# Kernel optimization log

Measured on AMD Instinct MI355X. Metric: run time of the kernel, lower is better.

The kernel has to match this reference:

```python
import jax, jax.numpy as jnp
import numpy as np

D_MODEL = 1024
D_HIDDEN = 4096
N_EXPERTS = 8
B, S = 2, 2048


def setup_inputs() -> dict:
    key = jax.random.key(0)
    ks = jax.random.split(key, 4)
    sd = 1.0 / np.sqrt(D_MODEL)
    sh = 1.0 / np.sqrt(D_HIDDEN)
    return {
        "x": jax.random.normal(ks[0], (B, S, D_MODEL), dtype=jnp.float32),
        "Wg": jax.random.normal(ks[1], (D_MODEL, N_EXPERTS), dtype=jnp.float32) * sd,
        "bg": jnp.zeros((N_EXPERTS,), dtype=jnp.float32),
        "W1": jax.random.normal(ks[2], (N_EXPERTS, D_MODEL, D_HIDDEN), dtype=jnp.float32) * sd,
        "b1": jnp.zeros((N_EXPERTS, D_HIDDEN), dtype=jnp.float32),
        "W2": jax.random.normal(ks[3], (N_EXPERTS, D_HIDDEN, D_MODEL), dtype=jnp.float32) * sh,
        "b2": jnp.zeros((N_EXPERTS, D_MODEL), dtype=jnp.float32),
    }


def reference(x, Wg, bg, W1, b1, W2, b2):
    # Router: softmax is monotone, so argmax(softmax(logits)) == argmax(logits).
    logits = jnp.einsum("bsd,de->bse", x, Wg) + bg
    expert_idx = jnp.argmax(logits, axis=-1)  # [B, S]
    # Top-1 dispatch, expressed as compute-all-experts + per-token select
    # (jit-friendly; the torch loop masks/gathers per expert).
    h = jax.nn.gelu(jnp.einsum("bsd,edh->bseh", x, W1) + b1, approximate=False)
    y = jnp.einsum("bseh,ehd->bsed", h, W2) + b2  # [B, S, E, D]
    out = jnp.take_along_axis(y, expert_idx[:, :, None, None], axis=2)[:, :, 0, :]
    return out
```

## Files before the change

kernel.cpp:

```cpp
#include <hip/hip_runtime.h>
#include <hip/hip_bf16.h>
#include <math.h>

#define D_MODEL 1024
#define D_HIDDEN 4096
#define N_EXP 8
#define N_TOK 4096
#define MBS2 24

typedef __attribute__((ext_vector_type(8))) __bf16 bf16x8_t;
typedef __attribute__((ext_vector_type(4))) float f32x4_t;

#define WS_PREFIX_OFF 128
#define WS_BUCKET_OFF 256
#define WS_HT_OFF     ((size_t)1 << 18)
#define WS_XB_OFF     ((size_t)1 << 18)
#define WS_HFB_OFF    (((size_t)1 << 18) + ((size_t)8 << 20))
#define WS_W1T_OFF    (((size_t)1 << 18) + ((size_t)48 << 20))
#define WS_W2T_OFF    (((size_t)1 << 18) + ((size_t)112 << 20))
#define WS_AE_OFF     (((size_t)1 << 18) + ((size_t)176 << 20))
#define WS_NEED       (((size_t)1 << 18) + ((size_t)188 << 20))

__device__ __forceinline__ void gload16(const void* g, void* l) {
    __builtin_amdgcn_global_load_lds(
        (__attribute__((address_space(1))) void*)(g),
        (__attribute__((address_space(3))) void*)(l),
        16, 0, 0);
}

__global__ __launch_bounds__(64) void init_counts(int* counts) {
    if (threadIdx.x < N_EXP) counts[threadIdx.x] = 0;
}

__global__ __launch_bounds__(64) void prefix_kernel(const int* counts, int* prefix) {
    if (threadIdx.x == 0) {
        int s = 0;
        prefix[0] = 0;
#pragma unroll
        for (int e = 0; e < N_EXP; ++e) { s += (counts[e] + 255) >> 8; prefix[e + 1] = s; }
    }
}

__global__ __launch_bounds__(256) void router_kernel(
    const float* __restrict__ x, const float* __restrict__ Wg,
    const float* __restrict__ bg, int* __restrict__ counts,
    int* __restrict__ bucket, __hip_bfloat16* __restrict__ xb)
{
    const int wid  = threadIdx.x >> 6;
    const int lane = threadIdx.x & 63;
    const int t    = blockIdx.x * 4 + wid;
    const float* xr = x + (size_t)t * D_MODEL;

    double acc[N_EXP];
#pragma unroll
    for (int e = 0; e < N_EXP; ++e) acc[e] = 0.0;

#pragma unroll
    for (int j = 0; j < D_MODEL / 64; ++j) {
        const int d = j * 64 + lane;
        const float xv = xr[d];
        xb[(size_t)t * D_MODEL + d] = __float2bfloat16(xv);
        const float4* wr = (const float4*)(Wg + (size_t)d * N_EXP);
        const float4 w0 = wr[0], w1 = wr[1];
        const double xd = (double)xv;
        acc[0] += xd * (double)w0.x; acc[1] += xd * (double)w0.y;
        acc[2] += xd * (double)w0.z; acc[3] += xd * (double)w0.w;
        acc[4] += xd * (double)w1.x; acc[5] += xd * (double)w1.y;
        acc[6] += xd * (double)w1.z; acc[7] += xd * (double)w1.w;
    }
#pragma unroll
    for (int e = 0; e < N_EXP; ++e) {
        double v = acc[e];
#pragma unroll
        for (int off = 32; off >= 1; off >>= 1) v += __shfl_xor(v, off, 64);
        acc[e] = v + (double)bg[e];
    }
    if (lane == 0) {
        int best = 0; double bv = acc[0];
#pragma unroll
        for (int e = 1; e < N_EXP; ++e)
            if (acc[e] > bv) { bv = acc[e]; best = e; }
        const int pos = atomicAdd(&counts[best], 1);
        bucket[best * N_TOK + pos] = t;
    }
}

template<int KT, int NT>
__global__ __launch_bounds__(256) void convert_w(
    const float* __restrict__ W, __hip_bfloat16* __restrict__ Wt)
{
    constexpr int NB = NT / 256, KC = KT / 64;
    const int nb128 = blockIdx.x, kc = blockIdx.y, e = blockIdx.z;
    const int k0 = kc * 64, n0 = nb128 * 128;
    const int nb = n0 >> 8, halfc = (n0 >> 7) & 1;
    const int tid = threadIdx.x;
    __shared__ __hip_bfloat16 Lt[128 * 68];

    const int nq  = tid & 31;
    const int kq2 = tid >> 5;
#pragma unroll
    for (int h = 0; h < 2; ++h) {
        const int kq = kq2 + h * 8;
        const float* src = W + (size_t)e * KT * NT + (size_t)(k0 + kq * 4) * NT + n0 + nq * 4;
        const float4 v0 = *(const float4*)(src);
        const float4 v1 = *(const float4*)(src + (size_t)NT);
        const float4 v2 = *(const float4*)(src + (size_t)2 * NT);
        const float4 v3 = *(const float4*)(src + (size_t)3 * NT);
#pragma unroll
        for (int i = 0; i < 4; ++i) {
            const int n = nq * 4 + i;
            union { __hip_bfloat16 hh[4]; unsigned long long u; } pk;
            pk.hh[0] = __float2bfloat16(((const float*)&v0)[i]);
            pk.hh[1] = __float2bfloat16(((const float*)&v1)[i]);
            pk.hh[2] = __float2bfloat16(((const float*)&v2)[i]);
            pk.hh[3] = __float2bfloat16(((const float*)&v3)[i]);
            *(unsigned long long*)((char*)Lt + (size_t)n * 136 + kq * 8) = pk.u;
        }
    }
    __syncthreads();

    char* outc = (char*)Wt + (((size_t)e * NB + nb) * KC + kc) * 32768 + halfc * 16384;
    const int n = tid >> 1, half = tid & 1;
#pragma unroll
    for (int s = 0; s < 4; ++s) {
        const int slot = half * 4 + s;
        const int ko = slot ^ (n & 7);
        const uint4 v = *(const uint4*)((const char*)Lt + (size_t)n * 136 + ko * 16);
        *(uint4*)(outc + (size_t)n * 128 + slot * 16) = v;
    }
}

__global__ __launch_bounds__(256) void gather_a(
    const float* __restrict__ x, const int* __restrict__ counts,
    const int* __restrict__ prefix, const int* __restrict__ bucket,
    __hip_bfloat16* __restrict__ Ae)
{
    const int mbg = blockIdx.x >> 1, halfm = blockIdx.x & 1, kc = blockIdx.y;
    if (mbg >= prefix[8]) return;
    int e = 0;
#pragma unroll
    for (int q = 1; q < 8; ++q) if (mbg >= prefix[q]) e = q;
    const int cnt  = counts[e];
    const int mblk = mbg - prefix[e];
    const int tid  = threadIdx.x;
    const int m = halfm * 128 + (tid >> 1);
    const int half = tid & 1;
    int idx = mblk * 256 + m;
    if (idx >= cnt) idx = cnt - 1;
    const int tok = bucket[e * N_TOK + idx];
    const float* src = x + (size_t)tok * D_MODEL + kc * 64 + half * 32;
    char* dst = (char*)Ae + ((size_t)mbg * 16 + kc) * 32768 + (size_t)m * 128;
#pragma unroll
    for (int s = 0; s < 4; ++s) {
        const float4 a = *(const float4*)(src + s * 8);
        const float4 b = *(const float4*)(src + s * 8 + 4);
        union { __hip_bfloat16 hh[8]; uint4 u; } pk;
#pragma unroll
        for (int j = 0; j < 4; ++j) {
            pk.hh[j]     = __float2bfloat16(((const float*)&a)[j]);
            pk.hh[j + 4] = __float2bfloat16(((const float*)&b)[j]);
        }
        const int ko = half * 4 + s;
        *(uint4*)(dst + ((ko ^ (m & 7)) << 4)) = pk.u;
    }
}

template<int K_TOT, int N_TOT, int SPLITS, bool IS_FFN1>
__global__ __launch_bounds__(512, 2) void ffn_gemm_q(
    const __hip_bfloat16* __restrict__ At,
    const __hip_bfloat16* __restrict__ Wt,
    const float* __restrict__ bias,
    const int* __restrict__ prefix,
    __hip_bfloat16* __restrict__ hout,
    float* __restrict__ pout)
{
    constexpr int KC     = K_TOT / 64;
    constexpr int KSTEPS = KC / SPLITS;
    constexpr int NB     = N_TOT / 256;
    constexpr int NWG    = NB * SPLITS * MBS2;

    const int orig = blockIdx.x;
    const int wg   = (orig & 7) * (NWG >> 3) + (orig >> 3);
    const int nblk = wg / (SPLITS * MBS2);
    const int r2   = wg % (SPLITS * MBS2);
    const int split = r2 / MBS2;
    const int mbg   = r2 % MBS2;
    if (mbg >= prefix[8]) return;
    int e = 0;
#pragma unroll
    for (int q = 1; q < 8; ++q) if (mbg >= prefix[q]) e = q;
    const int n0 = nblk * 256;

    const int tid  = threadIdx.x;
    const int lane = tid & 63;
    const int wid  = tid >> 6;
    const int wm   = wid >> 1, wn = wid & 1;

    __shared__ char As[2 * 32768];
    __shared__ char Bs[2 * 32768];

    const char* Ab = (const char*)At + ((size_t)mbg * KC + split * KSTEPS) * 32768;
    const char* Bb = (const char*)Wt + (((size_t)e * NB + nblk) * KC + split * KSTEPS) * 32768;
    const int off = wid * 4096 + lane * 16;
    char* lA = As + wid * 4096;
    char* lB = Bs + wid * 4096;

    f32x4_t acc[4][8];
#pragma unroll
    for (int f = 0; f < 4; ++f)
#pragma unroll
        for (int g = 0; g < 8; ++g) acc[f][g] = (f32x4_t){0.f, 0.f, 0.f, 0.f};

    {
        const char* Ac = Ab + off;
        const char* Bc = Bb + off;
#pragma unroll
        for (int i = 0; i < 4; ++i) gload16(Ac + i * 1024, lA + i * 1024);
#pragma unroll
        for (int i = 0; i < 4; ++i) gload16(Bc + i * 1024, lB + i * 1024);
    }
    asm volatile("s_waitcnt vmcnt(0)" ::: "memory");
    __builtin_amdgcn_s_barrier();
    __builtin_amdgcn_sched_barrier(0);

    for (int t = 0; t < KSTEPS; ++t) {
        const int c = t & 1;
        if (t + 1 < KSTEPS) {
            const char* Ac = Ab + (size_t)(t + 1) * 32768 + off;
            const char* Bc = Bb + (size_t)(t + 1) * 32768 + off;
            char* la = lA + (c ^ 1) * 32768;
            char* lb = lB + (c ^ 1) * 32768;
#pragma unroll
            for (int i = 0; i < 4; ++i) gload16(Ac + i * 1024, la + i * 1024);
#pragma unroll
            for (int i = 0; i < 4; ++i) gload16(Bc + i * 1024, lb + i * 1024);
        }
        __builtin_amdgcn_sched_barrier(0);

        const char* asb = As + c * 32768;
        const char* bsb = Bs + c * 32768;
#pragma unroll
        for (int kk = 0; kk < 2; ++kk) {
            uint4 af[4], bf[8];
            const int ko = kk * 4 + (lane >> 4);
#pragma unroll
            for (int f = 0; f < 4; ++f) {
                const int r = wm * 64 + f * 16 + (lane & 15);
                af[f] = *(const uint4*)(asb + r * 128 + ((ko ^ (r & 7)) << 4));
            }
#pragma unroll
            for (int g = 0; g < 8; ++g) {
                const int n = wn * 128 + g * 16 + (lane & 15);
                bf[g] = *(const uint4*)(bsb + n * 128 + ((ko ^ (n & 7)) << 4));
            }
#pragma unroll
            for (int f = 0; f < 4; ++f)
#pragma unroll
                for (int g = 0; g < 8; ++g)
                    acc[f][g] = __builtin_amdgcn_mfma_f32_16x16x32_bf16(
                        __builtin_bit_cast(bf16x8_t, af[f]),
                        __builtin_bit_cast(bf16x8_t, bf[g]),
                        acc[f][g], 0, 0, 0);
        }

        asm volatile("s_waitcnt vmcnt(0)" ::: "memory");
        __builtin_amdgcn_s_barrier();
        __builtin_amdgcn_sched_barrier(0);
    }

    if (IS_FFN1) {
        char* hb = (char*)hout + (size_t)mbg * (D_HIDDEN / 64) * 32768;
#pragma unroll
        for (int f = 0; f < 4; ++f) {
#pragma unroll
            for (int j = 0; j < 4; ++j) {
                const int m = wm * 64 + f * 16 + (lane >> 4) * 4 + j;
#pragma unroll
                for (int g = 0; g < 8; ++g) {
                    const int col = n0 + wn * 128 + g * 16 + (lane & 15);
                    float v = acc[f][g][j] + bias[e * N_TOT + col];
                    v = 0.5f * v * (1.0f + erff(v * 0.70710678118654752f));
                    const int kc = col >> 6, kw = col & 63, ko = kw >> 3, b = kw & 7;
                    *(__hip_bfloat16*)(hb + (size_t)kc * 32768 + (size_t)m * 128 +
                                       (((ko ^ (m & 7)) << 4) + (b << 1))) = __float2bfloat16(v);
                }
            }
        }
    } else {
        float* pb = pout + ((size_t)(split * MBS2 + mbg) * 256) * 1024;
#pragma unroll
        for (int f = 0; f < 4; ++f) {
#pragma unroll
            for (int j = 0; j < 4; ++j) {
                const int m = wm * 64 + f * 16 + (lane >> 4) * 4 + j;
#pragma unroll
                for (int g = 0; g < 8; ++g) {
                    const int col = n0 + wn * 128 + g * 16 + (lane & 15);
                    pb[(size_t)m * 1024 + col] = acc[f][g][j];
                }
            }
        }
    }
}

__global__ __launch_bounds__(256) void reduce_out(
    const float* __restrict__ P, const float* __restrict__ b2,
    const int* __restrict__ counts, const int* __restrict__ prefix,
    const int* __restrict__ bucket, float* __restrict__ out)
{
    const int slot = blockIdx.x;
    if (slot >= prefix[8]) return;
    int e = 0;
#pragma unroll
    for (int q = 1; q < 8; ++q) if (slot >= prefix[q]) e = q;
    const int cnt  = counts[e];
    const int mblk = slot - prefix[e];
    const int r    = blockIdx.y * 4 + (threadIdx.x >> 6);
    const int idx  = mblk * 256 + r;
    if (idx >= cnt) return;
    const int tok  = bucket[e * N_TOK + idx];
    const int lane = threadIdx.x & 63;
    const float* p0 = P + ((size_t)slot * 256 + r) * 1024;
    const float* p1 = P + ((size_t)(MBS2 + slot) * 256 + r) * 1024;
    const float* bb = b2 + e * 1024;
    float* op = out + (size_t)tok * 1024;
#pragma unroll
    for (int j = 0; j < 4; ++j) {
        const int c = j * 256 + lane * 4;
        const float4 a = *(const float4*)(p0 + c);
        const float4 b = *(const float4*)(p1 + c);
        const float4 w = *(const float4*)(bb + c);
        float4 v;
        v.x = a.x + b.x + w.x; v.y = a.y + b.y + w.y;
        v.z = a.z + b.z + w.z; v.w = a.w + b.w + w.w;
        *(float4*)(op + c) = v;
    }
}

template<int K_TOT, int N_TOT, bool IS_FFN1>
__global__ __launch_bounds__(256, 2) void ffn_gemm_f32(
    const __hip_bfloat16* __restrict__ A,
    const float* __restrict__ W,
    const float* __restrict__ bias,
    const int* __restrict__ counts,
    const int* __restrict__ bucket,
    __hip_bfloat16* __restrict__ hout,
    float* __restrict__ yout)
{
    const int e   = blockIdx.z;
    const int cnt = counts[e];
    const int m0  = blockIdx.y * 128;
    if (m0 >= cnt) return;
    const int n0   = blockIdx.x * 128;
    const int tid  = threadIdx.x;
    const int lane = tid & 63;
    const int wid  = tid >> 6;
    const int wm   = wid >> 1, wn = wid & 1;

    __shared__ __hip_bfloat16 As[128 * 64];
    __shared__ __hip_bfloat16 Bs[128 * 64];
    __shared__ int s_tok[128];

    if (tid < 128) {
        int idx = m0 + tid;
        if (idx >= cnt) idx = cnt - 1;
        s_tok[tid] = bucket[e * N_TOK + idx];
    }
    __syncthreads();

    const __hip_bfloat16* gA[4]; char* lA[4];
#pragma unroll
    for (int i = 0; i < 4; ++i) {
        const int r = wid * 32 + i * 8 + (lane >> 3);
        gA[i] = A + (size_t)s_tok[r] * K_TOT + (((lane & 7) ^ (r & 7)) << 3);
        lA[i] = (char*)As + (size_t)(wid * 32 + i * 8) * 128;
    }
    const int ko_t = lane & 7;
    const int nq   = wid * 8 + (lane >> 3);
    const float* wb = W + (size_t)e * K_TOT * N_TOT + (size_t)(ko_t * 8) * N_TOT + n0 + nq * 4;

    f32x4_t acc[4][4];
#pragma unroll
    for (int f = 0; f < 4; ++f)
#pragma unroll
        for (int g = 0; g < 4; ++g) acc[f][g] = (f32x4_t){0.f, 0.f, 0.f, 0.f};

    for (int k0 = 0; k0 < K_TOT; k0 += 64) {
#pragma unroll
        for (int i = 0; i < 4; ++i) gload16(gA[i] + k0, lA[i]);
        const float* wk = wb + (size_t)k0 * N_TOT;
        float4 v[8];
#pragma unroll
        for (int j = 0; j < 8; ++j) v[j] = *(const float4*)(wk + (size_t)j * N_TOT);
#pragma unroll
        for (int i = 0; i < 4; ++i) {
            const int n = nq * 4 + i;
            union { __hip_bfloat16 hh[8]; uint4 u; } pk;
#pragma unroll
            for (int j = 0; j < 8; ++j) pk.hh[j] = __float2bfloat16(((const float*)&v[j])[i]);
            *(uint4*)((char*)Bs + n * 128 + ((ko_t ^ (n & 7)) << 4)) = pk.u;
        }
        __syncthreads();

#pragma unroll
        for (int kk = 0; kk < 2; ++kk) {
            uint4 af[4], bf[4];
            const int ko = kk * 4 + (lane >> 4);
#pragma unroll
            for (int f = 0; f < 4; ++f) {
                const int r = wm * 64 + f * 16 + (lane & 15);
                af[f] = *(const uint4*)((const char*)As + r * 128 + ((ko ^ (r & 7)) << 4));
            }
#pragma unroll
            for (int g = 0; g < 4; ++g) {
                const int n = wn * 64 + g * 16 + (lane & 15);
                bf[g] = *(const uint4*)((const char*)Bs + n * 128 + ((ko ^ (n & 7)) << 4));
            }
#pragma unroll
            for (int f = 0; f < 4; ++f)
#pragma unroll
                for (int g = 0; g < 4; ++g)
                    acc[f][g] = __builtin_amdgcn_mfma_f32_16x16x32_bf16(
                        __builtin_bit_cast(bf16x8_t, af[f]),
                        __builtin_bit_cast(bf16x8_t, bf[g]),
                        acc[f][g], 0, 0, 0);
        }
        __syncthreads();
    }

#pragma unroll
    for (int f = 0; f < 4; ++f) {
#pragma unroll
        for (int j = 0; j < 4; ++j) {
            const int rl = wm * 64 + f * 16 + (lane >> 4) * 4 + j;
            const bool ok = (m0 + rl) < cnt;
            const int tok = s_tok[rl];
#pragma unroll
            for (int g = 0; g < 4; ++g) {
                const int col = n0 + wn * 64 + g * 16 + (lane & 15);
                float v = acc[f][g][j] + bias[e * N_TOT + col];
                if (IS_FFN1) {
                    v = 0.5f * v * (1.0f + erff(v * 0.70710678118654752f));
                    if (ok) hout[(size_t)tok * N_TOT + col] = __float2bfloat16(v);
                } else {
                    if (ok) yout[(size_t)tok * N_TOT + col] = v;
                }
            }
        }
    }
}

extern "C" void kernel_launch(void* const* d_in, const int* in_sizes, int n_in,
                              void* d_out, int out_size, void* d_ws, size_t ws_size,
                              hipStream_t stream) {
    const float* x  = (const float*)d_in[0];
    const float* Wg = (const float*)d_in[1];
    const float* bg = (const float*)d_in[2];
    const float* W1 = (const float*)d_in[3];
    const float* b1 = (const float*)d_in[4];
    const float* W2 = (const float*)d_in[5];
    const float* b2 = (const float*)d_in[6];
    float* out = (float*)d_out;

    char* ws = (char*)d_ws;
    int* counts = (int*)(ws);
    int* prefix = (int*)(ws + WS_PREFIX_OFF);
    int* bucket = (int*)(ws + WS_BUCKET_OFF);
    __hip_bfloat16* xb  = (__hip_bfloat16*)(ws + WS_XB_OFF);
    __hip_bfloat16* ht  = (__hip_bfloat16*)(ws + WS_HT_OFF);
    __hip_bfloat16* hfb = (__hip_bfloat16*)(ws + WS_HFB_OFF);
    __hip_bfloat16* w1t = (__hip_bfloat16*)(ws + WS_W1T_OFF);
    __hip_bfloat16* w2t = (__hip_bfloat16*)(ws + WS_W2T_OFF);
    __hip_bfloat16* ae  = (__hip_bfloat16*)(ws + WS_AE_OFF);
    float* partials     = (float*)(ws + WS_W1T_OFF);

    init_counts<<<dim3(1), dim3(64), 0, stream>>>(counts);
    router_kernel<<<dim3(N_TOK / 4), dim3(256), 0, stream>>>(x, Wg, bg, counts, bucket, xb);
    prefix_kernel<<<dim3(1), dim3(64), 0, stream>>>(counts, prefix);

    if (ws_size >= WS_NEED) {
        convert_w<D_MODEL, D_HIDDEN><<<dim3(32, 16, N_EXP), dim3(256), 0, stream>>>(W1, w1t);
        convert_w<D_HIDDEN, D_MODEL><<<dim3(8, 64, N_EXP), dim3(256), 0, stream>>>(W2, w2t);
        gather_a<<<dim3(MBS2 * 2, 16), dim3(256), 0, stream>>>(x, counts, prefix, bucket, ae);
        ffn_gemm_q<D_MODEL, D_HIDDEN, 1, true>
            <<<dim3(MBS2 * (D_HIDDEN / 256)), dim3(512), 0, stream>>>(
                ae, w1t, b1, prefix, ht, nullptr);
        ffn_gemm_q<D_HIDDEN, D_MODEL, 2, false>
            <<<dim3(MBS2 * (D_MODEL / 256) * 2), dim3(512), 0, stream>>>(
                ht, w2t, nullptr, prefix, nullptr, partials);
        reduce_out<<<dim3(MBS2, 64), dim3(256), 0, stream>>>(
            partials, b2, counts, prefix, bucket, out);
    } else {
        ffn_gemm_f32<D_MODEL, D_HIDDEN, true>
            <<<dim3(D_HIDDEN / 128, N_TOK / 128, N_EXP), dim3(256), 0, stream>>>(
                xb, W1, b1, counts, bucket, hfb, nullptr);
        ffn_gemm_f32<D_HIDDEN, D_MODEL, false>
            <<<dim3(D_MODEL / 128, N_TOK / 128, N_EXP), dim3(256), 0, stream>>>(
                hfb, W2, b2, counts, bucket, nullptr, out);
    }
}
```

Baseline: 354.8 us.

## Halve GEMM K-tile to 32 and raise occupancy to four blocks per CU

Changes the pre-tiled bf16 layout of the weights, the gathered activations and the hidden buffer from 64-wide to 32-wide K chunks, with a new 4-slot XOR swizzle. The GEMM now uses 64KB of LDS instead of 128KB and does one MFMA k-step per pipeline stage, and launch bounds ask for 4 blocks per CU instead of 2. The aim is more resident workgroups to hide memory latency. In exchange it adds twice as many barriers and waits per unit of K, and it may cause register spills under the tighter register budget with 32 accumulator vectors per thread.

```diff
diff --git a/kernel.cpp b/kernel.cpp
--- a/kernel.cpp
+++ b/kernel.cpp
@@ -89,10 +89,10 @@
 __global__ __launch_bounds__(256) void convert_w(
     const float* __restrict__ W, __hip_bfloat16* __restrict__ Wt)
 {
-    constexpr int NB = NT / 256, KC = KT / 64;
+    constexpr int NB = NT / 256, KC2 = KT / 32;
     const int nb128 = blockIdx.x, kc = blockIdx.y, e = blockIdx.z;
     const int k0 = kc * 64, n0 = nb128 * 128;
-    const int nb = n0 >> 8, halfc = (n0 >> 7) & 1;
+    const int nb = nb128 >> 1, roff = (nb128 & 1) * 128;
     const int tid = threadIdx.x;
     __shared__ __hip_bfloat16 Lt[128 * 68];
 
@@ -119,14 +119,14 @@
     }
     __syncthreads();
 
-    char* outc = (char*)Wt + (((size_t)e * NB + nb) * KC + kc) * 32768 + halfc * 16384;
     const int n = tid >> 1, half = tid & 1;
+    const int m = roff + n;
+    char* outc = (char*)Wt + (((size_t)e * NB + nb) * KC2 + kc * 2 + half) * 16384;
 #pragma unroll
     for (int s = 0; s < 4; ++s) {
-        const int slot = half * 4 + s;
-        const int ko = slot ^ (n & 7);
-        const uint4 v = *(const uint4*)((const char*)Lt + (size_t)n * 136 + ko * 16);
-        *(uint4*)(outc + (size_t)n * 128 + slot * 16) = v;
+        const int phys = s ^ ((m >> 1) & 3);
+        const uint4 v = *(const uint4*)((const char*)Lt + (size_t)n * 136 + half * 64 + s * 16);
+        *(uint4*)(outc + (size_t)m * 64 + phys * 16) = v;
     }
 }
 
@@ -149,7 +149,7 @@
     if (idx >= cnt) idx = cnt - 1;
     const int tok = bucket[e * N_TOK + idx];
     const float* src = x + (size_t)tok * D_MODEL + kc * 64 + half * 32;
-    char* dst = (char*)Ae + ((size_t)mbg * 16 + kc) * 32768 + (size_t)m * 128;
+    char* dst = (char*)Ae + ((size_t)mbg * 32 + kc * 2 + half) * 16384 + (size_t)m * 64;
 #pragma unroll
     for (int s = 0; s < 4; ++s) {
         const float4 a = *(const float4*)(src + s * 8);
@@ -160,13 +160,13 @@
             pk.hh[j]     = __float2bfloat16(((const float*)&a)[j]);
             pk.hh[j + 4] = __float2bfloat16(((const float*)&b)[j]);
         }
-        const int ko = half * 4 + s;
-        *(uint4*)(dst + ((ko ^ (m & 7)) << 4)) = pk.u;
+        const int phys = s ^ ((m >> 1) & 3);
+        *(uint4*)(dst + phys * 16) = pk.u;
     }
 }
 
 template<int K_TOT, int N_TOT, int SPLITS, bool IS_FFN1>
-__global__ __launch_bounds__(512, 2) void ffn_gemm_q(
+__global__ __launch_bounds__(512, 4) void ffn_gemm_q(
     const __hip_bfloat16* __restrict__ At,
     const __hip_bfloat16* __restrict__ Wt,
     const float* __restrict__ bias,
@@ -174,8 +174,8 @@
     __hip_bfloat16* __restrict__ hout,
     float* __restrict__ pout)
 {
-    constexpr int KC     = K_TOT / 64;
-    constexpr int KSTEPS = KC / SPLITS;
+    constexpr int KC2    = K_TOT / 32;
+    constexpr int KSTEPS = KC2 / SPLITS;
     constexpr int NB     = N_TOT / 256;
     constexpr int NWG    = NB * SPLITS * MBS2;
 
@@ -196,14 +196,14 @@
     const int wid  = tid >> 6;
     const int wm   = wid >> 1, wn = wid & 1;
 
-    __shared__ char As[2 * 32768];
-    __shared__ char Bs[2 * 32768];
-
-    const char* Ab = (const char*)At + ((size_t)mbg * KC + split * KSTEPS) * 32768;
-    const char* Bb = (const char*)Wt + (((size_t)e * NB + nblk) * KC + split * KSTEPS) * 32768;
-    const int off = wid * 4096 + lane * 16;
-    char* lA = As + wid * 4096;
-    char* lB = Bs + wid * 4096;
+    __shared__ char As[2 * 16384];
+    __shared__ char Bs[2 * 16384];
+
+    const char* Ab = (const char*)At + ((size_t)mbg * KC2 + split * KSTEPS) * 16384;
+    const char* Bb = (const char*)Wt + (((size_t)e * NB + nblk) * KC2 + split * KSTEPS) * 16384;
+    const int off = wid * 2048 + lane * 16;
+    char* lA = As + wid * 2048;
+    char* lB = Bs + wid * 2048;
 
     f32x4_t acc[4][8];
 #pragma unroll
@@ -214,10 +214,8 @@
     {
         const char* Ac = Ab + off;
         const char* Bc = Bb + off;
-#pragma unroll
-        for (int i = 0; i < 4; ++i) gload16(Ac + i * 1024, lA + i * 1024);
-#pragma unroll
-        for (int i = 0; i < 4; ++i) gload16(Bc + i * 1024, lB + i * 1024);
+        gload16(Ac, lA); gload16(Ac + 1024, lA + 1024);
+        gload16(Bc, lB); gload16(Bc + 1024, lB + 1024);
     }
     asm volatile("s_waitcnt vmcnt(0)" ::: "memory");
     __builtin_amdgcn_s_barrier();
@@ -226,42 +224,37 @@
     for (int t = 0; t < KSTEPS; ++t) {
         const int c = t & 1;
         if (t + 1 < KSTEPS) {
-            const char* Ac = Ab + (size_t)(t + 1) * 32768 + off;
-            const char* Bc = Bb + (size_t)(t + 1) * 32768 + off;
-            char* la = lA + (c ^ 1) * 32768;
-            char* lb = lB + (c ^ 1) * 32768;
-#pragma unroll
-            for (int i = 0; i < 4; ++i) gload16(Ac + i * 1024, la + i * 1024);
-#pragma unroll
-            for (int i = 0; i < 4; ++i) gload16(Bc + i * 1024, lb + i * 1024);
+            const char* Ac = Ab + (size_t)(t + 1) * 16384 + off;
+            const char* Bc = Bb + (size_t)(t + 1) * 16384 + off;
+            char* la = lA + (c ^ 1) * 16384;
+            char* lb = lB + (c ^ 1) * 16384;
+            gload16(Ac, la); gload16(Ac + 1024, la + 1024);
+            gload16(Bc, lb); gload16(Bc + 1024, lb + 1024);
         }
         __builtin_amdgcn_sched_barrier(0);
 
-        const char* asb = As + c * 32768;
-        const char* bsb = Bs + c * 32768;
-#pragma unroll
-        for (int kk = 0; kk < 2; ++kk) {
-            uint4 af[4], bf[8];
-            const int ko = kk * 4 + (lane >> 4);
-#pragma unroll
-            for (int f = 0; f < 4; ++f) {
-                const int r = wm * 64 + f * 16 + (lane & 15);
-                af[f] = *(const uint4*)(asb + r * 128 + ((ko ^ (r & 7)) << 4));
-            }
-#pragma unroll
-            for (int g = 0; g < 8; ++g) {
-                const int n = wn * 128 + g * 16 + (lane & 15);
-                bf[g] = *(const uint4*)(bsb + n * 128 + ((ko ^ (n & 7)) << 4));
-            }
-#pragma unroll
-            for (int f = 0; f < 4; ++f)
-#pragma unroll
-                for (int g = 0; g < 8; ++g)
-                    acc[f][g] = __builtin_amdgcn_mfma_f32_16x16x32_bf16(
-                        __builtin_bit_cast(bf16x8_t, af[f]),
-                        __builtin_bit_cast(bf16x8_t, bf[g]),
-                        acc[f][g], 0, 0, 0);
-        }
+        const char* asb = As + c * 16384;
+        const char* bsb = Bs + c * 16384;
+        uint4 af[4], bf[8];
+        const int ko = lane >> 4;
+#pragma unroll
+        for (int f = 0; f < 4; ++f) {
+            const int r = wm * 64 + f * 16 + (lane & 15);
+            af[f] = *(const uint4*)(asb + r * 64 + ((ko ^ ((r >> 1) & 3)) << 4));
+        }
+#pragma unroll
+        for (int g = 0; g < 8; ++g) {
+            const int n = wn * 128 + g * 16 + (lane & 15);
+            bf[g] = *(const uint4*)(bsb + n * 64 + ((ko ^ ((n >> 1) & 3)) << 4));
+        }
+#pragma unroll
+        for (int f = 0; f < 4; ++f)
+#pragma unroll
+            for (int g = 0; g < 8; ++g)
+                acc[f][g] = __builtin_amdgcn_mfma_f32_16x16x32_bf16(
+                    __builtin_bit_cast(bf16x8_t, af[f]),
+                    __builtin_bit_cast(bf16x8_t, bf[g]),
+                    acc[f][g], 0, 0, 0);
 
         asm volatile("s_waitcnt vmcnt(0)" ::: "memory");
         __builtin_amdgcn_s_barrier();
@@ -269,7 +262,7 @@
     }
 
     if (IS_FFN1) {
-        char* hb = (char*)hout + (size_t)mbg * (D_HIDDEN / 64) * 32768;
+        char* hb = (char*)hout + (size_t)mbg * (D_HIDDEN / 32) * 16384;
 #pragma unroll
         for (int f = 0; f < 4; ++f) {
 #pragma unroll
@@ -280,9 +273,9 @@
                     const int col = n0 + wn * 128 + g * 16 + (lane & 15);
                     float v = acc[f][g][j] + bias[e * N_TOT + col];
                     v = 0.5f * v * (1.0f + erff(v * 0.70710678118654752f));
-                    const int kc = col >> 6, kw = col & 63, ko = kw >> 3, b = kw & 7;
-                    *(__hip_bfloat16*)(hb + (size_t)kc * 32768 + (size_t)m * 128 +
-                                       (((ko ^ (m & 7)) << 4) + (b << 1))) = __float2bfloat16(v);
+                    const int kc2 = col >> 5, kw = col & 31, s = kw >> 3, b = kw & 7;
+                    *(__hip_bfloat16*)(hb + (size_t)kc2 * 16384 + (size_t)m * 64 +
+                                       (((s ^ ((m >> 1) & 3)) << 4) + (b << 1))) = __float2bfloat16(v);
                 }
             }
         }
```

Result: slower. 1.063 ms (+199.6%).
